# Kernel optimization log

Hardware: AMD Instinct MI355X
Metric: run time of the kernel (lower is better)

The kernel has to match this reference:

```python
import jax, jax.numpy as jnp
import numpy as np

N = 50000      # nodes
E = 800000     # edges
IN = 128       # in_dim
H = 8          # heads
C = 16         # h_dim (per-head out channels)
ED = 16        # edge_dim
G = 1000       # number of graphs
HC = H * C     # 128
EPS = 1e-16    # PyG softmax epsilon


def setup_inputs() -> dict:
    key = jax.random.key(0)
    ks = jax.random.split(key, 32)
    p = lambda i, shape: jax.random.normal(ks[i], shape, jnp.float32) * 0.1
    inp = {
        "x": jax.random.normal(ks[0], (N, IN), jnp.float32),
        "edge_index": jax.random.randint(ks[1], (2, E), 0, N),
        "edge_attr": jax.random.normal(ks[2], (E, ED), jnp.float32),
        "batch": jnp.sort(jax.random.randint(ks[3], (N,), 0, G)),
    }
    dims = [IN, HC, HC]
    for l in range(3):
        d = dims[l]
        inp[f"W{l+1}"] = p(4 + 6 * l, (d, HC))     # lin weight
        inp[f"We{l+1}"] = p(5 + 6 * l, (ED, HC))   # lin_edge weight
        inp[f"as{l+1}"] = p(6 + 6 * l, (H, C))     # att_src
        inp[f"ad{l+1}"] = p(7 + 6 * l, (H, C))     # att_dst
        inp[f"ae{l+1}"] = p(8 + 6 * l, (H, C))     # att_edge
        inp[f"b{l+1}"] = jnp.zeros((HC,), jnp.float32)
    D = 4 * HC  # cat(h1,h2,h3,h_pool_) -> 512
    inp["Wl1"] = p(22, (D, D)); inp["bl1"] = jnp.zeros((D,), jnp.float32)
    inp["Wl2"] = p(23, (D, 1)); inp["bl2"] = jnp.zeros((1,), jnp.float32)
    return inp


def gat_conv(x, src, dst, edge_attr, W, We, a_s, a_d, a_e, b):
    # x: [N, d_in] -> xs: [N, H, C]
    xs = (x @ W).reshape(-1, H, C)
    ea = (edge_attr @ We).reshape(-1, H, C)          # [E, H, C]
    al_src = jnp.sum(xs * a_s, axis=-1)              # [N, H]
    al_dst = jnp.sum(xs * a_d, axis=-1)              # [N, H]
    al_e = jnp.sum(ea * a_e, axis=-1)                # [E, H]
    alpha = al_src[src] + al_dst[dst] + al_e         # [E, H]
    alpha = jax.nn.leaky_relu(alpha, 0.2)
    amax = jax.ops.segment_max(alpha, dst, num_segments=N)
    ex = jnp.exp(alpha - amax[dst])
    denom = jax.ops.segment_sum(ex, dst, num_segments=N)
    alpha = ex / (denom[dst] + EPS)                  # softmax over in-edges of dst
    msg = xs[src] * alpha[..., None]                 # [E, H, C]
    out = jax.ops.segment_sum(msg, dst, num_segments=N)  # [N, H, C]
    return out.reshape(-1, HC) + b


def reference(x, edge_index, edge_attr, batch,
              W1, We1, as1, ad1, ae1, b1,
              W2, We2, as2, ad2, ae2, b2,
              W3, We3, as3, ad3, ae3, b3,
              Wl1, bl1, Wl2, bl2):
    src, dst = edge_index[0], edge_index[1]
    h1 = gat_conv(x, src, dst, edge_attr, W1, We1, as1, ad1, ae1, b1)
    h2 = gat_conv(h1, src, dst, edge_attr, W2, We2, as2, ad2, ae2, b2)
    h3 = gat_conv(h2, src, dst, edge_attr, W3, We3, as3, ad3, ae3, b3)
    # global_add_pool then broadcast back per node (vectorized gather,
    # replacing the original per-node python loop)
    h_pool = jax.ops.segment_sum(h3, batch, num_segments=G)   # [G, HC]
    h_pool_ = h_pool[batch]                                    # [N, HC]
    h = jnp.concatenate([h1, h2, h3, h_pool_], axis=1)         # [N, 4*HC]
    h = jax.nn.leaky_relu(h @ Wl1 + bl1, 0.01)
    return h @ Wl2 + bl2
```

## Files before the change

kernel.cpp:

```cpp
#include <hip/hip_runtime.h>

#define N_NODES 50000
#define N_EDGES 800000
#define N_GRAPH 1000

typedef short bf16x8 __attribute__((ext_vector_type(8)));
typedef float f32x4 __attribute__((ext_vector_type(4)));

__device__ inline short f2b(float f) {
    union { float f; unsigned u; } x; x.f = f;
    unsigned r = x.u + 0x7FFF + ((x.u >> 16) & 1);
    return (short)(r >> 16);
}
__device__ inline float b2f_lo(unsigned v) {
    union { unsigned u; float f; } x; x.u = v << 16; return x.f;
}
__device__ inline float b2f_hi(unsigned v) {
    union { unsigned u; float f; } x; x.u = v & 0xFFFF0000u; return x.f;
}
__device__ inline float b2f_s(short s) {
    union { unsigned u; float f; } x; x.u = ((unsigned)(unsigned short)s) << 16; return x.f;
}
__device__ inline unsigned pack2(short lo, short hi) {
    return ((unsigned)(unsigned short)lo) | (((unsigned)(unsigned short)hi) << 16);
}

__global__ void f2b_bulk(const float* __restrict__ in, short* __restrict__ out, int n4) {
    int t = blockIdx.x * blockDim.x + threadIdx.x;
    if (t >= n4) return;
    float4 v = *(const float4*)(in + (size_t)t * 4);
    *(short4*)(out + (size_t)t * 4) = make_short4(f2b(v.x), f2b(v.y), f2b(v.z), f2b(v.w));
}

__global__ void wbt_k(const float* __restrict__ W, short* __restrict__ WbT) {
    int idx = blockIdx.x * blockDim.x + threadIdx.x;
    int k = idx >> 7, c = idx & 127;
    WbT[(size_t)c * 128 + k] = f2b(W[idx]);
}

__global__ __launch_bounds__(256) void gemm_mfma(const short* __restrict__ Ab,
                                                 const short* __restrict__ WbT,
                                                 short* __restrict__ outb, int nrows) {
    const int tid = threadIdx.x;
    const int n0 = blockIdx.x * 64;
    const int wid = tid >> 6, lane = tid & 63;
    const int lr = lane & 15, kg = lane >> 4;
    const int wr = (wid >> 1) * 32;
    const int wc = (wid & 1) * 64;

    f32x4 acc[2][4] = {};

#pragma unroll
    for (int ks = 0; ks < 4; ks++) {
        const int k0 = ks * 32;
        bf16x8 a[2], b[4];
#pragma unroll
        for (int fm = 0; fm < 2; fm++) {
            int gr = n0 + wr + fm * 16 + lr;
            bf16x8 v = {};
            if (gr < nrows) v = *(const bf16x8*)(Ab + (size_t)gr * 128 + k0 + kg * 8);
            a[fm] = v;
        }
#pragma unroll
        for (int fn = 0; fn < 4; fn++)
            b[fn] = *(const bf16x8*)(WbT + (size_t)(wc + fn * 16 + lr) * 128 + k0 + kg * 8);
#pragma unroll
        for (int fm = 0; fm < 2; fm++)
#pragma unroll
            for (int fn = 0; fn < 4; fn++)
                acc[fm][fn] = __builtin_amdgcn_mfma_f32_16x16x32_bf16(
                    a[fm], b[fn], acc[fm][fn], 0, 0, 0);
    }
#pragma unroll
    for (int fm = 0; fm < 2; fm++) {
#pragma unroll
        for (int r = 0; r < 4; r++) {
            int gr = n0 + wr + fm * 16 + kg * 4 + r;
            if (gr < nrows) {
#pragma unroll
                for (int fn = 0; fn < 4; fn++) {
                    int col = wc + fn * 16 + lr;
                    outb[(size_t)gr * 128 + col] = f2b(acc[fm][fn][r]);
                }
            }
        }
    }
}

__global__ void node_al(const short* __restrict__ xsb, const float* __restrict__ a_s,
                        const float* __restrict__ a_d, float* __restrict__ alsrc,
                        float* __restrict__ aldst, int n) {
    int t = blockIdx.x * blockDim.x + threadIdx.x;
    if (t >= n * 8) return;
    int node = t >> 3, h = t & 7;
    const short* xp = xsb + (size_t)node * 128 + h * 16;
    uint4 u0 = *(const uint4*)(xp);
    uint4 u1 = *(const uint4*)(xp + 8);
    unsigned w[8] = {u0.x, u0.y, u0.z, u0.w, u1.x, u1.y, u1.z, u1.w};
    float ss = 0.f, dd = 0.f;
#pragma unroll
    for (int q = 0; q < 8; q++) {
        float lo = b2f_lo(w[q]), hi = b2f_hi(w[q]);
        ss += lo * a_s[h * 16 + q * 2] + hi * a_s[h * 16 + q * 2 + 1];
        dd += lo * a_d[h * 16 + q * 2] + hi * a_d[h * 16 + q * 2 + 1];
    }
    alsrc[t] = ss;
    aldst[t] = dd;
}

__global__ void hist_k(const int* __restrict__ ei, int* __restrict__ cnt, int ne) {
    int e = blockIdx.x * blockDim.x + threadIdx.x;
    if (e < ne) atomicAdd(&cnt[ei[ne + e]], 1);
}

__global__ void scan1_k(const int* __restrict__ cnt, int* __restrict__ rowptr,
                        int* __restrict__ part, int n) {
    __shared__ int s[256];
    int tid = threadIdx.x;
    int i = blockIdx.x * 256 + tid;
    int v = (i < n) ? cnt[i] : 0;
    s[tid] = v; __syncthreads();
#pragma unroll
    for (int off = 1; off < 256; off <<= 1) {
        int t = (tid >= off) ? s[tid - off] : 0;
        __syncthreads();
        s[tid] += t;
        __syncthreads();
    }
    if (i < n) rowptr[i] = s[tid] - v;
    if (tid == 255) part[blockIdx.x] = s[255];
}

__global__ void scan2_k(int* __restrict__ part, int npart) {
    __shared__ int s[256];
    int tid = threadIdx.x;
    int v = (tid < npart) ? part[tid] : 0;
    s[tid] = v; __syncthreads();
#pragma unroll
    for (int off = 1; off < 256; off <<= 1) {
        int t = (tid >= off) ? s[tid - off] : 0;
        __syncthreads();
        s[tid] += t;
        __syncthreads();
    }
    if (tid < npart) part[tid] = s[tid] - v;
}

__global__ void scan3_k(int* __restrict__ rowptr, const int* __restrict__ part,
                        int* __restrict__ cursor, int n, int ne) {
    int i = blockIdx.x * 256 + threadIdx.x;
    if (i < n) {
        int r = rowptr[i] + part[blockIdx.x];
        rowptr[i] = r;
        cursor[i] = r;
    }
    if (i == 0) rowptr[n] = ne;
}

__global__ void scatter_k(const int* __restrict__ ei, int* __restrict__ cursor,
                          int* __restrict__ pos, int* __restrict__ csr_src, int ne) {
    int e = blockIdx.x * blockDim.x + threadIdx.x;
    if (e >= ne) return;
    int d = ei[ne + e];
    int p = atomicAdd(&cursor[d], 1);
    pos[e] = p;
    csr_src[p] = ei[e];
}

__global__ __launch_bounds__(256) void ale_k(const int* __restrict__ ei,
                                             const float* __restrict__ eattr,
                                             const float* __restrict__ alsrc,
                                             const float* __restrict__ We,
                                             const float* __restrict__ ae,
                                             const int* __restrict__ pos,
                                             short* __restrict__ aleb, int ne) {
    __shared__ float sAe[128];
    if (threadIdx.x < 128) {
        int k = threadIdx.x >> 3, h = threadIdx.x & 7;
        float s = 0.f;
#pragma unroll
        for (int c = 0; c < 16; c++) s += We[k * 128 + h * 16 + c] * ae[h * 16 + c];
        sAe[threadIdx.x] = s;
    }
    __syncthreads();
    int e = blockIdx.x * blockDim.x + threadIdx.x;
    if (e >= ne) return;
    float ea[16];
    const float4* ep = (const float4*)(eattr + (size_t)e * 16);
#pragma unroll
    for (int q = 0; q < 4; q++) {
        float4 v = ep[q];
        ea[q * 4 + 0] = v.x; ea[q * 4 + 1] = v.y; ea[q * 4 + 2] = v.z; ea[q * 4 + 3] = v.w;
    }
    int s = ei[e];
    float out[8];
#pragma unroll
    for (int h = 0; h < 8; h++) out[h] = alsrc[s * 8 + h];
#pragma unroll
    for (int k = 0; k < 16; k++)
#pragma unroll
        for (int h = 0; h < 8; h++) out[h] += ea[k] * sAe[k * 8 + h];
    short v8[8];
#pragma unroll
    for (int h = 0; h < 8; h++) v8[h] = f2b(out[h]);
    short* op = aleb + (size_t)pos[e] * 8;
    *(short4*)(op)     = make_short4(v8[0], v8[1], v8[2], v8[3]);
    *(short4*)(op + 4) = make_short4(v8[4], v8[5], v8[6], v8[7]);
}

__global__ __launch_bounds__(256) void gather_k(const int* __restrict__ rowptr,
                                                const int* __restrict__ csr_src,
                                                const short* __restrict__ aleb,
                                                const float* __restrict__ aldst,
                                                const short* __restrict__ xsb,
                                                const float* __restrict__ b,
                                                short* __restrict__ houtb, int n) {
    int dst = blockIdx.x * 4 + (threadIdx.x >> 6);
    if (dst >= n) return;
    const int lane = threadIdx.x & 63;
    const int h = lane >> 3;
    const float L2E = 1.44269504f;
    int p0 = rowptr[dst], p1 = rowptr[dst + 1];
    float ald = aldst[dst * 8 + h];
    float den = 0.f, acc0 = 0.f, acc1 = 0.f;
    int p = p0;
    const int nfull = (p1 - p0) >> 3;
    int   sv  = 0;
    float alv = 0.f;
    if (nfull > 0) {
        sv  = csr_src[p + (lane & 7)];
        alv = b2f_s(aleb[(size_t)p * 8 + lane]);
    }
    for (int c = 0; c < nfull; c++) {
        int csv = sv; float calv = alv;
        int pn = p + 8;
        if (c + 1 < nfull) {
            sv  = csr_src[pn + (lane & 7)];
            alv = b2f_s(aleb[(size_t)pn * 8 + lane]);
        }
        int s0 = __shfl(csv, 0), s1 = __shfl(csv, 1), s2 = __shfl(csv, 2), s3 = __shfl(csv, 3);
        int s4 = __shfl(csv, 4), s5 = __shfl(csv, 5), s6 = __shfl(csv, 6), s7 = __shfl(csv, 7);
        unsigned v0 = *(const unsigned*)(xsb + (size_t)s0 * 128 + lane * 2);
        unsigned v1 = *(const unsigned*)(xsb + (size_t)s1 * 128 + lane * 2);
        unsigned v2 = *(const unsigned*)(xsb + (size_t)s2 * 128 + lane * 2);
        unsigned v3 = *(const unsigned*)(xsb + (size_t)s3 * 128 + lane * 2);
        unsigned v4 = *(const unsigned*)(xsb + (size_t)s4 * 128 + lane * 2);
        unsigned v5 = *(const unsigned*)(xsb + (size_t)s5 * 128 + lane * 2);
        unsigned v6 = *(const unsigned*)(xsb + (size_t)s6 * 128 + lane * 2);
        unsigned v7 = *(const unsigned*)(xsb + (size_t)s7 * 128 + lane * 2);
        unsigned vv[8] = {v0, v1, v2, v3, v4, v5, v6, v7};
#pragma unroll
        for (int i = 0; i < 8; i++) {
            float al = __shfl(calv, i * 8 + h);
            float lg = al + ald; lg = lg > 0.f ? lg : 0.2f * lg;
            float ex = exp2f(lg * L2E);
            den  += ex;
            acc0 += b2f_lo(vv[i]) * ex;
            acc1 += b2f_hi(vv[i]) * ex;
        }
        p = pn;
    }
    for (; p + 1 < p1; p += 2) {
        int s0 = csr_src[p];
        int s1 = csr_src[p + 1];
        float al0 = b2f_s(aleb[(size_t)p * 8 + h]);
        float al1 = b2f_s(aleb[(size_t)(p + 1) * 8 + h]);
        unsigned v0 = *(const unsigned*)(xsb + (size_t)s0 * 128 + lane * 2);
        unsigned v1 = *(const unsigned*)(xsb + (size_t)s1 * 128 + lane * 2);
        float lg0 = al0 + ald; lg0 = lg0 > 0.f ? lg0 : 0.2f * lg0;
        float lg1 = al1 + ald; lg1 = lg1 > 0.f ? lg1 : 0.2f * lg1;
        float ex0 = exp2f(lg0 * L2E);
        float ex1 = exp2f(lg1 * L2E);
        den  += ex0 + ex1;
        acc0 += b2f_lo(v0) * ex0 + b2f_lo(v1) * ex1;
        acc1 += b2f_hi(v0) * ex0 + b2f_hi(v1) * ex1;
    }
    if (p < p1) {
        int s0 = csr_src[p];
        float al0 = b2f_s(aleb[(size_t)p * 8 + h]);
        unsigned v0 = *(const unsigned*)(xsb + (size_t)s0 * 128 + lane * 2);
        float lg0 = al0 + ald; lg0 = lg0 > 0.f ? lg0 : 0.2f * lg0;
        float ex0 = exp2f(lg0 * L2E);
        den  += ex0;
        acc0 += b2f_lo(v0) * ex0;
        acc1 += b2f_hi(v0) * ex0;
    }
    float inv = 1.f / (den + 1e-16f);
    const float2 bb = *(const float2*)(b + lane * 2);
    unsigned o = pack2(f2b(acc0 * inv + bb.x), f2b(acc1 * inv + bb.y));
    *(unsigned*)(houtb + (size_t)dst * 128 + lane * 2) = o;
}

__global__ void pool_k(const short* __restrict__ h3b, const int* __restrict__ batch,
                       float* __restrict__ pool, int n) {
    int t = blockIdx.x * blockDim.x + threadIdx.x;
    if (t >= n * 128) return;
    int node = t >> 7, j = t & 127;
    atomicAdd(pool + (size_t)batch[node] * 128 + j, b2f_s(h3b[t]));
}

__global__ void wl1t_k(const float* __restrict__ Wl1, short* __restrict__ Wl1T) {
    int idx = blockIdx.x * blockDim.x + threadIdx.x;
    int k = idx >> 9, c = idx & 511;
    Wl1T[(size_t)c * 512 + k] = f2b(Wl1[idx]);
}

__global__ void init_out(float* __restrict__ out, const float* __restrict__ bl2, int n) {
    int t = blockIdx.x * blockDim.x + threadIdx.x;
    if (t < n) out[t] = bl2[0];
}

__global__ __launch_bounds__(256) void final_mfma(
    const short* __restrict__ h1, const short* __restrict__ h2,
    const short* __restrict__ h3, const short* __restrict__ poolb,
    const int* __restrict__ batch, const short* __restrict__ Wl1T,
    const float* __restrict__ bl1, const float* __restrict__ Wl2,
    float* __restrict__ out, int nrows)
{
    __shared__ short Abuf[2][4 * 64 * 8];
    __shared__ int   sBatch[64];
    const int tid = threadIdx.x;
    const int n0 = blockIdx.x * 64;
    const int j0 = blockIdx.y * 256;
    const int wid = tid >> 6, lane = tid & 63;
    const int lr = lane & 15, kg = lane >> 4;

    if (tid < 64) {
        int gr = n0 + tid;
        sBatch[tid] = (gr < nrows) ? batch[gr] : 0;
    }
    __syncthreads();

    const short* seg_base[4] = {h1, h2, h3, poolb};

    auto STAGE = [&](int t) {
        const int k0 = t * 32;
        const int seg = k0 >> 7;
        const short* base = seg_base[seg];
        const int cseg = k0 & 127;
        int gr = n0 + lane;
        int grow = (seg == 3) ? sBatch[lane] : ((gr < nrows) ? gr : 0);
        const short* src = base + (size_t)grow * 128 + cseg + wid * 8;
#if __has_builtin(__builtin_amdgcn_global_load_lds)
        __builtin_amdgcn_global_load_lds(
            (const __attribute__((address_space(1))) unsigned int*)src,
            (__attribute__((address_space(3))) unsigned int*)&Abuf[t & 1][(wid * 64 + lane) * 8],
            16, 0, 0);
#else
        uint4 v = *(const uint4*)src;
        *(uint4*)(&Abuf[t & 1][(wid * 64 + lane) * 8]) = v;
#endif
    };
    auto LOADB = [&](int t, bf16x8* bb) {
        const int k0 = t * 32;
#pragma unroll
        for (int fn = 0; fn < 4; fn++)
            bb[fn] = *(const bf16x8*)(Wl1T + (size_t)(j0 + wid * 64 + fn * 16 + lr) * 512
                                      + k0 + kg * 8);
    };

    f32x4 acc[4][4] = {};
    bf16x8 bc[4], bn[4];

    STAGE(0);
    LOADB(0, bc);
    __syncthreads();
#pragma unroll
    for (int t = 0; t < 16; t++) {
        if (t < 15) {
            STAGE(t + 1);
            LOADB(t + 1, bn);
        }
        bf16x8 a[4];
#pragma unroll
        for (int fm = 0; fm < 4; fm++)
            a[fm] = *(const bf16x8*)(&Abuf[t & 1][(kg * 64 + fm * 16 + lr) * 8]);
#pragma unroll
        for (int fm = 0; fm < 4; fm++)
#pragma unroll
            for (int fn = 0; fn < 4; fn++)
                acc[fm][fn] = __builtin_amdgcn_mfma_f32_16x16x32_bf16(
                    a[fm], bc[fn], acc[fm][fn], 0, 0, 0);
        if (t < 15) {
            __syncthreads();
#pragma unroll
            for (int fn = 0; fn < 4; fn++) bc[fn] = bn[fn];
        }
    }

    float w2[4], b1c[4];
#pragma unroll
    for (int fn = 0; fn < 4; fn++) {
        int c = j0 + wid * 64 + fn * 16 + lr;
        w2[fn]  = Wl2[c];
        b1c[fn] = bl1[c];
    }

#pragma unroll
    for (int fm = 0; fm < 4; fm++) {
#pragma unroll
        for (int r = 0; r < 4; r++) {
            float s = 0.f;
#pragma unroll
            for (int fn = 0; fn < 4; fn++) {
                float z = acc[fm][fn][r] + b1c[fn];
                z = z > 0.f ? z : 0.01f * z;
                s += z * w2[fn];
            }
            s += __shfl_xor(s, 1);
            s += __shfl_xor(s, 2);
            s += __shfl_xor(s, 4);
            s += __shfl_xor(s, 8);
            if (lr == 0) {
                int gr = n0 + fm * 16 + kg * 4 + r;
                if (gr < nrows) atomicAdd(out + gr, s);
            }
        }
    }
}

extern "C" void kernel_launch(void* const* d_in, const int* in_sizes, int n_in,
                              void* d_out, int out_size, void* d_ws, size_t ws_size,
                              hipStream_t stream) {
    const float* x     = (const float*)d_in[0];
    const int*   ei    = (const int*)d_in[1];
    const float* eattr = (const float*)d_in[2];
    const int*   batch = (const int*)d_in[3];
    const float* W[3]   = {(const float*)d_in[4],  (const float*)d_in[10], (const float*)d_in[16]};
    const float* We[3]  = {(const float*)d_in[5],  (const float*)d_in[11], (const float*)d_in[17]};
    const float* as_[3] = {(const float*)d_in[6],  (const float*)d_in[12], (const float*)d_in[18]};
    const float* ad_[3] = {(const float*)d_in[7],  (const float*)d_in[13], (const float*)d_in[19]};
    const float* ae_[3] = {(const float*)d_in[8],  (const float*)d_in[14], (const float*)d_in[20]};
    const float* b_[3]  = {(const float*)d_in[9],  (const float*)d_in[15], (const float*)d_in[21]};
    const float* Wl1 = (const float*)d_in[22];
    const float* bl1 = (const float*)d_in[23];
    const float* Wl2 = (const float*)d_in[24];
    const float* bl2 = (const float*)d_in[25];

    const int N = N_NODES, E = N_EDGES, G = N_GRAPH;

    float* ws    = (float*)d_ws;
    float* alsrc = ws;
    float* aldst = alsrc + (size_t)N * 8;
    float* pool  = aldst + (size_t)N * 8;
    short* xb    = (short*)(pool + (size_t)G * 128);
    short* xsb   = xb + (size_t)N * 128;
    short* hb0   = xsb + (size_t)N * 128;
    short* hb1   = hb0 + (size_t)N * 128;
    short* hb2   = hb1 + (size_t)N * 128;
    short* hb[3] = {hb0, hb1, hb2};
    short* poolb = hb2 + (size_t)N * 128;
    short* wbt0  = poolb + (size_t)G * 128;
    short* wbt1  = wbt0 + 16384;
    short* wbt2  = wbt1 + 16384;
    short* wbt[3] = {wbt0, wbt1, wbt2};
    short* wl1t  = wbt2 + 16384;
    short* aleb  = wl1t + 262144;
    int*   cnt     = (int*)(aleb + (size_t)E * 8);
    int*   rowptr  = cnt + N;
    int*   cursor  = rowptr + N + 1;
    int*   part    = cursor + N;
    int*   pos     = part + 256;
    int*   csr_src = pos + E;

    f2b_bulk<<<(N * 32 + 255) / 256, 256, 0, stream>>>(x, xb, N * 32);
    for (int l = 0; l < 3; l++)
        wbt_k<<<64, 256, 0, stream>>>(W[l], wbt[l]);
    wl1t_k<<<1024, 256, 0, stream>>>(Wl1, wl1t);
    hipMemsetAsync(cnt, 0, (size_t)N * sizeof(int), stream);
    hist_k<<<(E + 255) / 256, 256, 0, stream>>>(ei, cnt, E);
    const int nblk = (N + 255) / 256;
    scan1_k<<<nblk, 256, 0, stream>>>(cnt, rowptr, part, N);
    scan2_k<<<1, 256, 0, stream>>>(part, nblk);
    scan3_k<<<nblk, 256, 0, stream>>>(rowptr, part, cursor, N, E);
    scatter_k<<<(E + 255) / 256, 256, 0, stream>>>(ei, cursor, pos, csr_src, E);

    for (int l = 0; l < 3; l++) {
        const short* Ain = (l == 0) ? xb : hb[l - 1];
        gemm_mfma<<<(N + 63) / 64, 256, 0, stream>>>(Ain, wbt[l], xsb, N);
        node_al<<<(N * 8 + 255) / 256, 256, 0, stream>>>(xsb, as_[l], ad_[l], alsrc, aldst, N);
        ale_k<<<(E + 255) / 256, 256, 0, stream>>>(ei, eattr, alsrc, We[l], ae_[l],
                                                   pos, aleb, E);
        gather_k<<<(N + 3) / 4, 256, 0, stream>>>(rowptr, csr_src, aleb, aldst, xsb,
                                                  b_[l], hb[l], N);
    }
    hipMemsetAsync(pool, 0, (size_t)G * 128 * sizeof(float), stream);
    pool_k<<<(N * 128 + 255) / 256, 256, 0, stream>>>(hb[2], batch, pool, N);
    f2b_bulk<<<(G * 32 + 255) / 256, 256, 0, stream>>>(pool, poolb, G * 32);

    init_out<<<(N + 255) / 256, 256, 0, stream>>>((float*)d_out, bl2, N);
    dim3 fg((N + 63) / 64, 2);
    final_mfma<<<fg, 256, 0, stream>>>(hb[0], hb[1], hb[2], poolb, batch,
                                       wl1t, bl1, Wl2, (float*)d_out, N);
}
```

Baseline: 482.2 us.

## Pad CSR rows to multiples of eight and pre-permute edge attributes

Each destination's CSR segment is rounded up to a multiple of 8, and the padding slots are marked with a negative source index. The edge-logit kernel writes a large negative value for those slots so their softmax weight becomes negligible, which lets the gather kernel drop its scalar tail loops and run only the 8-wide chunked path. Edge attributes are converted to bf16 and scattered into CSR order once, so the per-layer ale kernel reads them contiguously, with no pos indirection and no fp32 edge reads. The cost is extra padded work (up to 8*N slots), an additional memset, and clamped gathers of node 0 for the padding entries.

Result: faster. 453.7 us (-5.9%).

```diff
diff --git a/kernel.cpp b/kernel.cpp
--- a/kernel.cpp
+++ b/kernel.cpp
@@ -3,6 +3,7 @@
 #define N_NODES 50000
 #define N_EDGES 800000
 #define N_GRAPH 1000
+#define EPAD (N_EDGES + 8 * N_NODES)
 
 typedef short bf16x8 __attribute__((ext_vector_type(8)));
 typedef float f32x4 __attribute__((ext_vector_type(4)));
@@ -118,7 +119,7 @@
     __shared__ int s[256];
     int tid = threadIdx.x;
     int i = blockIdx.x * 256 + tid;
-    int v = (i < n) ? cnt[i] : 0;
+    int v = (i < n) ? ((cnt[i] + 7) & ~7) : 0;
     s[tid] = v; __syncthreads();
 #pragma unroll
     for (int off = 1; off < 256; off <<= 1) {
@@ -147,33 +148,39 @@
 }
 
 __global__ void scan3_k(int* __restrict__ rowptr, const int* __restrict__ part,
-                        int* __restrict__ cursor, int n, int ne) {
+                        const int* __restrict__ cnt, int* __restrict__ cursor, int n) {
     int i = blockIdx.x * 256 + threadIdx.x;
     if (i < n) {
         int r = rowptr[i] + part[blockIdx.x];
         rowptr[i] = r;
         cursor[i] = r;
-    }
-    if (i == 0) rowptr[n] = ne;
-}
-
-__global__ void scatter_k(const int* __restrict__ ei, int* __restrict__ cursor,
-                          int* __restrict__ pos, int* __restrict__ csr_src, int ne) {
+        if (i == n - 1) rowptr[n] = r + ((cnt[i] + 7) & ~7);
+    }
+}
+
+__global__ void scatter_k(const int* __restrict__ ei, const float* __restrict__ eattr,
+                          int* __restrict__ cursor, int* __restrict__ csr_src,
+                          short* __restrict__ eatb, int ne) {
     int e = blockIdx.x * blockDim.x + threadIdx.x;
     if (e >= ne) return;
     int d = ei[ne + e];
     int p = atomicAdd(&cursor[d], 1);
-    pos[e] = p;
     csr_src[p] = ei[e];
-}
-
-__global__ __launch_bounds__(256) void ale_k(const int* __restrict__ ei,
-                                             const float* __restrict__ eattr,
+    const float4* ep = (const float4*)(eattr + (size_t)e * 16);
+    short* op = eatb + (size_t)p * 16;
+#pragma unroll
+    for (int q = 0; q < 4; q++) {
+        float4 v = ep[q];
+        *(short4*)(op + q * 4) = make_short4(f2b(v.x), f2b(v.y), f2b(v.z), f2b(v.w));
+    }
+}
+
+__global__ __launch_bounds__(256) void ale_k(const int* __restrict__ csr_src,
+                                             const short* __restrict__ eatb,
                                              const float* __restrict__ alsrc,
                                              const float* __restrict__ We,
                                              const float* __restrict__ ae,
-                                             const int* __restrict__ pos,
-                                             short* __restrict__ aleb, int ne) {
+                                             short* __restrict__ aleb, int ntot) {
     __shared__ float sAe[128];
     if (threadIdx.x < 128) {
         int k = threadIdx.x >> 3, h = threadIdx.x & 7;
@@ -184,18 +191,26 @@
     }
     __syncthreads();
     int e = blockIdx.x * blockDim.x + threadIdx.x;
-    if (e >= ne) return;
+    if (e >= ntot) return;
+    int s = csr_src[e];
+    short* op = aleb + (size_t)e * 8;
+    if (s < 0) {
+        short m = f2b(-300.f);
+        *(short4*)(op)     = make_short4(m, m, m, m);
+        *(short4*)(op + 4) = make_short4(m, m, m, m);
+        return;
+    }
+    uint4 u0 = *(const uint4*)(eatb + (size_t)e * 16);
+    uint4 u1 = *(const uint4*)(eatb + (size_t)e * 16 + 8);
+    unsigned w[8] = {u0.x, u0.y, u0.z, u0.w, u1.x, u1.y, u1.z, u1.w};
     float ea[16];
-    const float4* ep = (const float4*)(eattr + (size_t)e * 16);
-#pragma unroll
-    for (int q = 0; q < 4; q++) {
-        float4 v = ep[q];
-        ea[q * 4 + 0] = v.x; ea[q * 4 + 1] = v.y; ea[q * 4 + 2] = v.z; ea[q * 4 + 3] = v.w;
-    }
-    int s = ei[e];
+#pragma unroll
+    for (int q = 0; q < 8; q++) { ea[q * 2] = b2f_lo(w[q]); ea[q * 2 + 1] = b2f_hi(w[q]); }
     float out[8];
-#pragma unroll
-    for (int h = 0; h < 8; h++) out[h] = alsrc[s * 8 + h];
+    const float4* ap = (const float4*)(alsrc + (size_t)s * 8);
+    float4 a0 = ap[0], a1 = ap[1];
+    out[0] = a0.x; out[1] = a0.y; out[2] = a0.z; out[3] = a0.w;
+    out[4] = a1.x; out[5] = a1.y; out[6] = a1.z; out[7] = a1.w;
 #pragma unroll
     for (int k = 0; k < 16; k++)
 #pragma unroll
@@ -203,7 +218,6 @@
     short v8[8];
 #pragma unroll
     for (int h = 0; h < 8; h++) v8[h] = f2b(out[h]);
-    short* op = aleb + (size_t)pos[e] * 8;
     *(short4*)(op)     = make_short4(v8[0], v8[1], v8[2], v8[3]);
     *(short4*)(op + 4) = make_short4(v8[4], v8[5], v8[6], v8[7]);
 }
@@ -223,8 +237,8 @@
     int p0 = rowptr[dst], p1 = rowptr[dst + 1];
     float ald = aldst[dst * 8 + h];
     float den = 0.f, acc0 = 0.f, acc1 = 0.f;
+    const int nfull = (p1 - p0) >> 3;
     int p = p0;
-    const int nfull = (p1 - p0) >> 3;
     int   sv  = 0;
     float alv = 0.f;
     if (nfull > 0) {
@@ -240,6 +254,10 @@
         }
         int s0 = __shfl(csv, 0), s1 = __shfl(csv, 1), s2 = __shfl(csv, 2), s3 = __shfl(csv, 3);
         int s4 = __shfl(csv, 4), s5 = __shfl(csv, 5), s6 = __shfl(csv, 6), s7 = __shfl(csv, 7);
+        s0 = s0 < 0 ? 0 : s0;  s1 = s1 < 0 ? 0 : s1;
+        s2 = s2 < 0 ? 0 : s2;  s3 = s3 < 0 ? 0 : s3;
+        s4 = s4 < 0 ? 0 : s4;  s5 = s5 < 0 ? 0 : s5;
+        s6 = s6 < 0 ? 0 : s6;  s7 = s7 < 0 ? 0 : s7;
         unsigned v0 = *(const unsigned*)(xsb + (size_t)s0 * 128 + lane * 2);
         unsigned v1 = *(const unsigned*)(xsb + (size_t)s1 * 128 + lane * 2);
         unsigned v2 = *(const unsigned*)(xsb + (size_t)s2 * 128 + lane * 2);
@@ -259,31 +277,6 @@
             acc1 += b2f_hi(vv[i]) * ex;
         }
         p = pn;
-    }
-    for (; p + 1 < p1; p += 2) {
-        int s0 = csr_src[p];
-        int s1 = csr_src[p + 1];
-        float al0 = b2f_s(aleb[(size_t)p * 8 + h]);
-        float al1 = b2f_s(aleb[(size_t)(p + 1) * 8 + h]);
-        unsigned v0 = *(const unsigned*)(xsb + (size_t)s0 * 128 + lane * 2);
-        unsigned v1 = *(const unsigned*)(xsb + (size_t)s1 * 128 + lane * 2);
-        float lg0 = al0 + ald; lg0 = lg0 > 0.f ? lg0 : 0.2f * lg0;
-        float lg1 = al1 + ald; lg1 = lg1 > 0.f ? lg1 : 0.2f * lg1;
-        float ex0 = exp2f(lg0 * L2E);
-        float ex1 = exp2f(lg1 * L2E);
-        den  += ex0 + ex1;
-        acc0 += b2f_lo(v0) * ex0 + b2f_lo(v1) * ex1;
-        acc1 += b2f_hi(v0) * ex0 + b2f_hi(v1) * ex1;
-    }
-    if (p < p1) {
-        int s0 = csr_src[p];
-        float al0 = b2f_s(aleb[(size_t)p * 8 + h]);
-        unsigned v0 = *(const unsigned*)(xsb + (size_t)s0 * 128 + lane * 2);
-        float lg0 = al0 + ald; lg0 = lg0 > 0.f ? lg0 : 0.2f * lg0;
-        float ex0 = exp2f(lg0 * L2E);
-        den  += ex0;
-        acc0 += b2f_lo(v0) * ex0;
-        acc1 += b2f_hi(v0) * ex0;
     }
     float inv = 1.f / (den + 1e-16f);
     const float2 bb = *(const float2*)(b + lane * 2);
@@ -456,31 +449,32 @@
     short* wbt[3] = {wbt0, wbt1, wbt2};
     short* wl1t  = wbt2 + 16384;
     short* aleb  = wl1t + 262144;
-    int*   cnt     = (int*)(aleb + (size_t)E * 8);
+    short* eatb  = aleb + (size_t)EPAD * 8;
+    int*   cnt     = (int*)(eatb + (size_t)EPAD * 16);
     int*   rowptr  = cnt + N;
     int*   cursor  = rowptr + N + 1;
     int*   part    = cursor + N;
-    int*   pos     = part + 256;
-    int*   csr_src = pos + E;
+    int*   csr_src = part + 256;
 
     f2b_bulk<<<(N * 32 + 255) / 256, 256, 0, stream>>>(x, xb, N * 32);
     for (int l = 0; l < 3; l++)
         wbt_k<<<64, 256, 0, stream>>>(W[l], wbt[l]);
     wl1t_k<<<1024, 256, 0, stream>>>(Wl1, wl1t);
     hipMemsetAsync(cnt, 0, (size_t)N * sizeof(int), stream);
+    hipMemsetAsync(csr_src, 0x80, (size_t)EPAD * sizeof(int), stream);
     hist_k<<<(E + 255) / 256, 256, 0, stream>>>(ei, cnt, E);
     const int nblk = (N + 255) / 256;
     scan1_k<<<nblk, 256, 0, stream>>>(cnt, rowptr, part, N);
     scan2_k<<<1, 256, 0, stream>>>(part, nblk);
-    scan3_k<<<nblk, 256, 0, stream>>>(rowptr, part, cursor, N, E);
-    scatter_k<<<(E + 255) / 256, 256, 0, stream>>>(ei, cursor, pos, csr_src, E);
-
+    scan3_k<<<nblk, 256, 0, stream>>>(rowptr, part, cnt, cursor, N);
+    scatter_k<<<(E + 255) / 256, 256, 0, stream>>>(ei, eattr, cursor, csr_src, eatb, E);
+
+    const int aleGrid = (EPAD + 255) / 256;
     for (int l = 0; l < 3; l++) {
         const short* Ain = (l == 0) ? xb : hb[l - 1];
         gemm_mfma<<<(N + 63) / 64, 256, 0, stream>>>(Ain, wbt[l], xsb, N);
         node_al<<<(N * 8 + 255) / 256, 256, 0, stream>>>(xsb, as_[l], ad_[l], alsrc, aldst, N);
-        ale_k<<<(E + 255) / 256, 256, 0, stream>>>(ei, eattr, alsrc, We[l], ae_[l],
-                                                   pos, aleb, E);
+        ale_k<<<aleGrid, 256, 0, stream>>>(csr_src, eatb, alsrc, We[l], ae_[l], aleb, EPAD);
         gather_k<<<(N + 3) / 4, 256, 0, stream>>>(rowptr, csr_src, aleb, aldst, xsb,
                                                   b_[l], hb[l], N);
     }
```
